# Optimization experiments

Measured on AMD Instinct MI355X. Metric: run time of the kernel, lower is better.

## Reference

```python
import jax, jax.numpy as jnp
import numpy as np


def dct_matrix(N, dtype=jnp.float32):
    # DCT-II orthonormal basis: D[k, n] = s_k * cos(pi * (n + 0.5) * k / N)
    n = jnp.arange(N, dtype=dtype)
    k = jnp.arange(N, dtype=dtype)
    M = jnp.cos(jnp.pi * (n[None, :] + 0.5) * k[:, None] / N)
    scale = jnp.full((N,), jnp.sqrt(2.0 / N), dtype=dtype).at[0].set(jnp.sqrt(1.0 / N))
    return scale[:, None] * M  # [K, N]


def setup_inputs() -> dict:
    key = jax.random.key(0)
    k1, k2, k3, k4 = jax.random.split(key, 4)
    B, C, H, W = 64, 3, 512, 512
    x = jax.random.normal(k1, (B, C, H, W), dtype=jnp.float32)
    attention = jax.random.uniform(k2, (H, W), dtype=jnp.float32)
    row_weights = jax.random.uniform(k3, (H,), dtype=jnp.float32)
    col_weights = jax.random.uniform(k4, (W,), dtype=jnp.float32)
    return {"x": x, "attention": attention, "row_weights": row_weights,
            "col_weights": col_weights}


def reference(x, attention, row_weights, col_weights):
    B, C, H, W = x.shape
    Dw = dct_matrix(W, x.dtype)  # DCT along last axis
    Dh = dct_matrix(H, x.dtype)  # DCT along second-to-last axis
    # dct(x, axis=-1): contract columns; dct(., axis=-2): contract rows
    x_dct = jnp.einsum('kh,bchw,lw->bckl', Dh, x, Dw)
    gray = x_dct.mean(axis=1)                 # [B, H, W]
    weighted = gray * attention               # [B, H, W]
    row_sum = weighted.mean(axis=2)           # [B, H]
    col_sum = weighted.mean(axis=1)           # [B, W]
    row_output = (row_sum * row_weights).mean(axis=1)  # [B]
    col_output = (col_sum * col_weights).mean(axis=1)  # [B]
    return jax.nn.sigmoid(jnp.stack([col_output, row_output], axis=1))  # [B, 2]
```

## Files before the change

### kernel.cpp

```cpp
#include <hip/hip_runtime.h>
#include <hip/hip_bf16.h>
#include <math.h>


typedef __attribute__((ext_vector_type(8))) short bf16x8;
typedef __attribute__((ext_vector_type(4))) float f32x4;

#define NFULL 512
#define HWTOT 262144
#define SCALE_M (1.0f / 786432.0f)
#define KC_BLOCKS 2048

static __device__ __forceinline__ unsigned short f_to_bf16(float f) {
  union { float f; unsigned int i; } v; v.f = f;
  unsigned int r = v.i + 0x7FFFu + ((v.i >> 16) & 1u);
  return (unsigned short)(r >> 16);
}
static __device__ __forceinline__ float bf_lo(unsigned int u) {
  union { unsigned int i; float f; } v; v.i = u << 16; return v.f;
}
static __device__ __forceinline__ float bf_hi(unsigned int u) {
  union { unsigned int i; float f; } v; v.i = u & 0xFFFF0000u; return v.f;
}

__global__ void k0_prep(const float* __restrict__ att,
                        const float* __restrict__ rw,
                        const float* __restrict__ cw,
                        unsigned short* __restrict__ DT,
                        unsigned short* __restrict__ Arw,
                        unsigned short* __restrict__ Acw) {
  int idx = blockIdx.x * blockDim.x + threadIdx.x;
  int r = idx >> 9;
  int c = idx & 511;
  unsigned int ph = ((unsigned int)(2 * r + 1) * (unsigned int)c) & 2047u;
  float s = (c == 0) ? 0.04419417382415922f
                     : 0.0625f;
  DT[idx] = f_to_bf16(s * cospif((float)ph * (1.0f / 1024.0f)));
  float a = att[idx];
  Arw[idx] = f_to_bf16(a * rw[r]);
  Acw[idx] = f_to_bf16(a * cw[c]);
}

__global__ __launch_bounds__(256) void ka_gemm(const unsigned short* __restrict__ DT,
                                               const unsigned short* __restrict__ Arw,
                                               const unsigned short* __restrict__ Acw,
                                               unsigned short* __restrict__ T1T,
                                               unsigned short* __restrict__ T2T) {
  __shared__ f32x4 r1[4][64];
  __shared__ f32x4 r2[4][64];
  int tile = blockIdx.x;
  int tk = tile >> 5, tw = tile & 31;
  int tid = threadIdx.x, lane = tid & 63, wv = tid >> 6;
  int row_a = tk * 16 + (lane & 15);
  int row_b = tw * 16 + (lane & 15);
  int koff = (lane >> 4) * 8;
  int l0beg = wv * 128;

  const bf16x8* A1 = (const bf16x8*)(Arw + row_a * NFULL);
  const bf16x8* A2 = (const bf16x8*)(Acw + row_a * NFULL);
  const bf16x8* Bp = (const bf16x8*)(DT  + row_b * NFULL);

  f32x4 acc1 = {0.f, 0.f, 0.f, 0.f};
  f32x4 acc2 = {0.f, 0.f, 0.f, 0.f};
#pragma unroll
  for (int l0 = 0; l0 < 128; l0 += 32) {
    int e = (l0beg + l0 + koff) >> 3;
    bf16x8 b = Bp[e];
    acc1 = __builtin_amdgcn_mfma_f32_16x16x32_bf16(A1[e], b, acc1, 0, 0, 0);
    acc2 = __builtin_amdgcn_mfma_f32_16x16x32_bf16(A2[e], b, acc2, 0, 0, 0);
  }
  r1[wv][lane] = acc1;
  r2[wv][lane] = acc2;
  __syncthreads();
  if (wv == 0) {
    f32x4 s1 = (r1[0][lane] + r1[1][lane]) + (r1[2][lane] + r1[3][lane]);
    f32x4 s2 = (r2[0][lane] + r2[1][lane]) + (r2[2][lane] + r2[3][lane]);
    int col = lane & 15, r0 = (lane >> 4) * 4;
    int w  = tw * 16 + col;
    int k0 = tk * 16 + r0;
    unsigned int g0 = f_to_bf16(s1[0]) | ((unsigned int)f_to_bf16(s1[1]) << 16);
    unsigned int g1 = f_to_bf16(s1[2]) | ((unsigned int)f_to_bf16(s1[3]) << 16);
    unsigned int c0 = f_to_bf16(s2[0]) | ((unsigned int)f_to_bf16(s2[1]) << 16);
    unsigned int c1 = f_to_bf16(s2[2]) | ((unsigned int)f_to_bf16(s2[3]) << 16);
    *(uint2*)(T1T + w * NFULL + k0) = make_uint2(g0, g1);
    *(uint2*)(T2T + w * NFULL + k0) = make_uint2(c0, c1);
  }
}

__global__ __launch_bounds__(256) void kb_gemm(const unsigned short* __restrict__ DT,
                                               const unsigned short* __restrict__ T1T,
                                               const unsigned short* __restrict__ T2T,
                                               unsigned int* __restrict__ Mpk) {
  __shared__ f32x4 r1[4][64];
  __shared__ f32x4 r2[4][64];
  int tile = blockIdx.x;
  int th = tile >> 5, tw = tile & 31;
  int tid = threadIdx.x, lane = tid & 63, wv = tid >> 6;
  int row_a = th * 16 + (lane & 15);
  int row_b = tw * 16 + (lane & 15);
  int koff = (lane >> 4) * 8;
  int k0beg = wv * 128;

  const bf16x8* Ap = (const bf16x8*)(DT  + row_a * NFULL);
  const bf16x8* Rp = (const bf16x8*)(T1T + row_b * NFULL);
  const bf16x8* Cp = (const bf16x8*)(T2T + row_b * NFULL);

  f32x4 accR = {0.f, 0.f, 0.f, 0.f};
  f32x4 accC = {0.f, 0.f, 0.f, 0.f};
#pragma unroll
  for (int k0 = 0; k0 < 128; k0 += 32) {
    int e = (k0beg + k0 + koff) >> 3;
    bf16x8 a = Ap[e];
    accR = __builtin_amdgcn_mfma_f32_16x16x32_bf16(a, Rp[e], accR, 0, 0, 0);
    accC = __builtin_amdgcn_mfma_f32_16x16x32_bf16(a, Cp[e], accC, 0, 0, 0);
  }
  r1[wv][lane] = accR;
  r2[wv][lane] = accC;
  __syncthreads();
  if (wv == 0) {
    f32x4 sR = (r1[0][lane] + r1[1][lane]) + (r1[2][lane] + r1[3][lane]);
    f32x4 sC = (r2[0][lane] + r2[1][lane]) + (r2[2][lane] + r2[3][lane]);
    int col = lane & 15, r0 = (lane >> 4) * 4;
    int h0 = th * 16 + r0;
    int w  = tw * 16 + col;
#pragma unroll
    for (int j = 0; j < 4; ++j) {
      Mpk[(h0 + j) * NFULL + w] =
          (unsigned int)f_to_bf16(sC[j] * SCALE_M) |
          ((unsigned int)f_to_bf16(sR[j] * SCALE_M) << 16);
    }
  }
}

__global__ __launch_bounds__(256, 6) void kc_dot(const float* __restrict__ x,
                                                 const unsigned int* __restrict__ Mpk,
                                                 float* __restrict__ partial) {
  int b   = blockIdx.x >> 5;
  int sub = blockIdx.x & 31;
  int tid = threadIdx.x;
  const f32x4* __restrict__ xp = (const f32x4*)x + (size_t)b * 196608;
  const uint4* __restrict__ mp4 = (const uint4*)Mpk;

  int base = sub * 2048 + tid;

  uint4 mp[3];
  f32x4 xs0[3], xs1[3], xs2[3];
#define LOADIT(s, it)                                   \
  {                                                     \
    int i_ = base + (it) * 256;                         \
    mp[s]  = mp4[i_];                                   \
    xs0[s] = xp[i_];                                    \
    xs1[s] = xp[i_ + 65536];                            \
    xs2[s] = xp[i_ + 131072];                           \
  }
  LOADIT(0, 0)
  LOADIT(1, 1)
  LOADIT(2, 2)

  float a0 = 0.f, a1 = 0.f;
#pragma unroll
  for (int it = 0; it < 8; ++it) {
    int s = it % 3;
    f32x4 sv = (xs0[s] + xs1[s]) + xs2[s];
    uint4 m = mp[s];
    if (it + 3 < 8) LOADIT(s, it + 3)
    a0 += sv.x * bf_lo(m.x) + sv.y * bf_lo(m.y) + sv.z * bf_lo(m.z) + sv.w * bf_lo(m.w);
    a1 += sv.x * bf_hi(m.x) + sv.y * bf_hi(m.y) + sv.z * bf_hi(m.z) + sv.w * bf_hi(m.w);
  }
#undef LOADIT

  int lane = tid & 63, wv = tid >> 6;
#pragma unroll
  for (int off = 32; off > 0; off >>= 1) {
    a0 += __shfl_down(a0, off);
    a1 += __shfl_down(a1, off);
  }
  __shared__ float red[8];
  if (lane == 0) { red[wv * 2] = a0; red[wv * 2 + 1] = a1; }
  __syncthreads();
  if (tid == 0) {
    float s0 = red[0] + red[2] + red[4] + red[6];
    float s1 = red[1] + red[3] + red[5] + red[7];
    partial[(b * 32 + sub) * 2 + 0] = s0;
    partial[(b * 32 + sub) * 2 + 1] = s1;
  }
}

__global__ void kd_final(const float* __restrict__ partial, float* __restrict__ out) {
  int t = threadIdx.x;
  int b = t >> 1, o = t & 1;
  float s = 0.f;
#pragma unroll
  for (int j = 0; j < 32; ++j) s += partial[(b * 32 + j) * 2 + o];
  out[b * 2 + o] = 1.0f / (1.0f + expf(-s));
}

extern "C" void kernel_launch(void* const* d_in, const int* in_sizes, int n_in,
                              void* d_out, int out_size, void* d_ws, size_t ws_size,
                              hipStream_t stream) {
  const float* x   = (const float*)d_in[0];
  const float* att = (const float*)d_in[1];
  const float* rw  = (const float*)d_in[2];
  const float* cw  = (const float*)d_in[3];
  float* out = (float*)d_out;

  unsigned short* DT  = (unsigned short*)d_ws;
  unsigned short* Arw = DT  + HWTOT;
  unsigned short* Acw = Arw + HWTOT;
  unsigned short* T1T = Acw + HWTOT;
  unsigned short* T2T = T1T + HWTOT;
  unsigned int*  Mpk  = (unsigned int*)(T2T + HWTOT);
  float* partial = (float*)(Mpk + HWTOT);

  k0_prep<<<1024, 256, 0, stream>>>(att, rw, cw, DT, Arw, Acw);
  ka_gemm<<<1024, 256, 0, stream>>>(DT, Arw, Acw, T1T, T2T);
  kb_gemm<<<1024, 256, 0, stream>>>(DT, T1T, T2T, Mpk);
  kc_dot<<<KC_BLOCKS, 256, 0, stream>>>(x, Mpk, partial);
  kd_final<<<1, 128, 0, stream>>>(partial, out);
}
```

Baseline: 56.97 us.

## Fuse prep kernel into GEMMs by computing DCT and attention fragments inline

Removes the separate prep kernel that materialised the DCT matrix and the attention-times-weight bf16 matrices in workspace. The first GEMM now loads attention and column weights directly and builds the bf16 operands in registers. Both GEMMs compute DCT basis fragments on the fly with cospif. This saves one launch and the round-trip through global memory, at the cost of redundant transcendental work in every tile.

```diff
diff --git a/kernel.cpp b/kernel.cpp
--- a/kernel.cpp
+++ b/kernel.cpp
@@ -10,6 +10,8 @@
 #define HWTOT 262144
 #define SCALE_M (1.0f / 786432.0f)
 #define KC_BLOCKS 2048
+#define S0 0.04419417382415922f
+#define S1 0.0625f
 
 static __device__ __forceinline__ unsigned short f_to_bf16(float f) {
   union { float f; unsigned int i; } v; v.f = f;
@@ -23,51 +25,56 @@
   union { unsigned int i; float f; } v; v.i = u & 0xFFFF0000u; return v.f;
 }
 
-__global__ void k0_prep(const float* __restrict__ att,
-                        const float* __restrict__ rw,
-                        const float* __restrict__ cw,
-                        unsigned short* __restrict__ DT,
-                        unsigned short* __restrict__ Arw,
-                        unsigned short* __restrict__ Acw) {
-  int idx = blockIdx.x * blockDim.x + threadIdx.x;
-  int r = idx >> 9;
-  int c = idx & 511;
-  unsigned int ph = ((unsigned int)(2 * r + 1) * (unsigned int)c) & 2047u;
-  float s = (c == 0) ? 0.04419417382415922f
-                     : 0.0625f;
-  DT[idx] = f_to_bf16(s * cospif((float)ph * (1.0f / 1024.0f)));
-  float a = att[idx];
-  Arw[idx] = f_to_bf16(a * rw[r]);
-  Acw[idx] = f_to_bf16(a * cw[c]);
-}
-
-__global__ __launch_bounds__(256) void ka_gemm(const unsigned short* __restrict__ DT,
-                                               const unsigned short* __restrict__ Arw,
-                                               const unsigned short* __restrict__ Acw,
-                                               unsigned short* __restrict__ T1T,
-                                               unsigned short* __restrict__ T2T) {
+static __device__ __forceinline__ bf16x8 dct_frag(int r, int cbase) {
+  unsigned int st = (unsigned int)(2 * r + 1);
+  unsigned int pb = st * (unsigned int)cbase;
+  bf16x8 v;
+#pragma unroll
+  for (int j = 0; j < 8; ++j) {
+    unsigned int ph = (pb + (unsigned int)j * st) & 2047u;
+    float s = ((cbase + j) == 0) ? S0 : S1;
+    v[j] = (short)f_to_bf16(s * cospif((float)ph * (1.0f / 1024.0f)));
+  }
+  return v;
+}
+
+__global__ __launch_bounds__(256) void ka2(const float* __restrict__ att,
+                                           const float* __restrict__ rw,
+                                           const float* __restrict__ cw,
+                                           unsigned short* __restrict__ T1T,
+                                           unsigned short* __restrict__ T2T) {
   __shared__ f32x4 r1[4][64];
   __shared__ f32x4 r2[4][64];
   int tile = blockIdx.x;
   int tk = tile >> 5, tw = tile & 31;
   int tid = threadIdx.x, lane = tid & 63, wv = tid >> 6;
-  int row_a = tk * 16 + (lane & 15);
-  int row_b = tw * 16 + (lane & 15);
+  int l16 = lane & 15;
   int koff = (lane >> 4) * 8;
+  int row_a = tk * 16 + l16;
+  int row_b = tw * 16 + l16;
   int l0beg = wv * 128;
-
-  const bf16x8* A1 = (const bf16x8*)(Arw + row_a * NFULL);
-  const bf16x8* A2 = (const bf16x8*)(Acw + row_a * NFULL);
-  const bf16x8* Bp = (const bf16x8*)(DT  + row_b * NFULL);
+  float rwa = rw[row_a];
 
   f32x4 acc1 = {0.f, 0.f, 0.f, 0.f};
   f32x4 acc2 = {0.f, 0.f, 0.f, 0.f};
 #pragma unroll
   for (int l0 = 0; l0 < 128; l0 += 32) {
-    int e = (l0beg + l0 + koff) >> 3;
-    bf16x8 b = Bp[e];
-    acc1 = __builtin_amdgcn_mfma_f32_16x16x32_bf16(A1[e], b, acc1, 0, 0, 0);
-    acc2 = __builtin_amdgcn_mfma_f32_16x16x32_bf16(A2[e], b, acc2, 0, 0, 0);
+    int cbase = l0beg + l0 + koff;
+    const f32x4* ap = (const f32x4*)(att + row_a * NFULL + cbase);
+    f32x4 av0 = ap[0], av1 = ap[1];
+    const f32x4* cp = (const f32x4*)(cw + cbase);
+    f32x4 cw0 = cp[0], cw1 = cp[1];
+    bf16x8 a1, a2;
+    float av[8] = {av0.x, av0.y, av0.z, av0.w, av1.x, av1.y, av1.z, av1.w};
+    float cv[8] = {cw0.x, cw0.y, cw0.z, cw0.w, cw1.x, cw1.y, cw1.z, cw1.w};
+#pragma unroll
+    for (int j = 0; j < 8; ++j) {
+      a1[j] = (short)f_to_bf16(av[j] * rwa);
+      a2[j] = (short)f_to_bf16(av[j] * cv[j]);
+    }
+    bf16x8 b = dct_frag(row_b, cbase);
+    acc1 = __builtin_amdgcn_mfma_f32_16x16x32_bf16(a1, b, acc1, 0, 0, 0);
+    acc2 = __builtin_amdgcn_mfma_f32_16x16x32_bf16(a2, b, acc2, 0, 0, 0);
   }
   r1[wv][lane] = acc1;
   r2[wv][lane] = acc2;
@@ -87,21 +94,20 @@
   }
 }
 
-__global__ __launch_bounds__(256) void kb_gemm(const unsigned short* __restrict__ DT,
-                                               const unsigned short* __restrict__ T1T,
-                                               const unsigned short* __restrict__ T2T,
-                                               unsigned int* __restrict__ Mpk) {
+__global__ __launch_bounds__(256) void kb2(const unsigned short* __restrict__ T1T,
+                                           const unsigned short* __restrict__ T2T,
+                                           unsigned int* __restrict__ Mpk) {
   __shared__ f32x4 r1[4][64];
   __shared__ f32x4 r2[4][64];
   int tile = blockIdx.x;
   int th = tile >> 5, tw = tile & 31;
   int tid = threadIdx.x, lane = tid & 63, wv = tid >> 6;
-  int row_a = th * 16 + (lane & 15);
-  int row_b = tw * 16 + (lane & 15);
+  int l16 = lane & 15;
   int koff = (lane >> 4) * 8;
+  int row_a = th * 16 + l16;
+  int row_b = tw * 16 + l16;
   int k0beg = wv * 128;
 
-  const bf16x8* Ap = (const bf16x8*)(DT  + row_a * NFULL);
   const bf16x8* Rp = (const bf16x8*)(T1T + row_b * NFULL);
   const bf16x8* Cp = (const bf16x8*)(T2T + row_b * NFULL);
 
@@ -109,8 +115,9 @@
   f32x4 accC = {0.f, 0.f, 0.f, 0.f};
 #pragma unroll
   for (int k0 = 0; k0 < 128; k0 += 32) {
-    int e = (k0beg + k0 + koff) >> 3;
-    bf16x8 a = Ap[e];
+    int cbase = k0beg + k0 + koff;
+    int e = cbase >> 3;
+    bf16x8 a = dct_frag(row_a, cbase);
     accR = __builtin_amdgcn_mfma_f32_16x16x32_bf16(a, Rp[e], accR, 0, 0, 0);
     accC = __builtin_amdgcn_mfma_f32_16x16x32_bf16(a, Cp[e], accC, 0, 0, 0);
   }
@@ -204,17 +211,13 @@
   const float* cw  = (const float*)d_in[3];
   float* out = (float*)d_out;
 
-  unsigned short* DT  = (unsigned short*)d_ws;
-  unsigned short* Arw = DT  + HWTOT;
-  unsigned short* Acw = Arw + HWTOT;
-  unsigned short* T1T = Acw + HWTOT;
+  unsigned short* T1T = (unsigned short*)d_ws;
   unsigned short* T2T = T1T + HWTOT;
   unsigned int*  Mpk  = (unsigned int*)(T2T + HWTOT);
   float* partial = (float*)(Mpk + HWTOT);
 
-  k0_prep<<<1024, 256, 0, stream>>>(att, rw, cw, DT, Arw, Acw);
-  ka_gemm<<<1024, 256, 0, stream>>>(DT, Arw, Acw, T1T, T2T);
-  kb_gemm<<<1024, 256, 0, stream>>>(DT, T1T, T2T, Mpk);
+  ka2<<<1024, 256, 0, stream>>>(att, rw, cw, T1T, T2T);
+  kb2<<<1024, 256, 0, stream>>>(T1T, T2T, Mpk);
   kc_dot<<<KC_BLOCKS, 256, 0, stream>>>(x, Mpk, partial);
   kd_final<<<1, 128, 0, stream>>>(partial, out);
 }
```

Measured after the change: 57.75 us. No clear change (+1.4%).
